# Performance work log

Hardware: AMD Instinct MI355X
Metric: run time of the kernel (lower is better)

## Reference

```python
import jax, jax.numpy as jnp
import numpy as np
import math

B, N, D, H, E, EDGE_DIM, GEO_DIM = 32, 256, 512, 8, 1024, 256, 64
HD = D // H

def _lin(x, W, b):
    return x @ W.T + b

def _ln(x, g, b):
    m = x.mean(-1, keepdims=True)
    v = ((x - m) ** 2).mean(-1, keepdims=True)
    return (x - m) * jax.lax.rsqrt(v + 1e-5) * g + b

def setup_inputs() -> dict:
    key = jax.random.key(0)
    ks = jax.random.split(key, 20)
    p = lambda k, s: jax.random.normal(k, s, jnp.float32) * 0.02
    inp = {
        'x': jax.random.normal(ks[0], (B, N, D), jnp.float32),
        'node_masks': jnp.ones((B, N), jnp.float32),
        'relation_edges': jax.random.randint(ks[1], (B, E, 2), 0, N),
        'relation_masks': (jax.random.uniform(ks[2], (B, E)) > 0.2).astype(jnp.float32),
        'relation_embeddings': jax.random.normal(ks[3], (B, E, EDGE_DIM), jnp.float32),
        'relation_geo_features': jax.random.normal(ks[4], (B, E, GEO_DIM), jnp.float32),
        'Wq': p(ks[5], (D, D)), 'bq': jnp.zeros((D,), jnp.float32),
        'Wk': p(ks[6], (D, D)), 'bk': jnp.zeros((D,), jnp.float32),
        'Wv': p(ks[7], (D, D)), 'bv': jnp.zeros((D,), jnp.float32),
        'W_eb': p(ks[8], (H, EDGE_DIM)), 'b_eb': jnp.zeros((H,), jnp.float32),
        'geo_ln_g': jnp.ones((GEO_DIM,), jnp.float32), 'geo_ln_b': jnp.zeros((GEO_DIM,), jnp.float32),
        'W_geo': p(ks[9], (H, GEO_DIM)), 'b_geo': jnp.zeros((H,), jnp.float32),
        'W_out': p(ks[10], (D, D)), 'b_out': jnp.zeros((D,), jnp.float32),
        'norm_g': jnp.ones((D,), jnp.float32), 'norm_b': jnp.zeros((D,), jnp.float32),
        'ff_ln_g': jnp.ones((D,), jnp.float32), 'ff_ln_b': jnp.zeros((D,), jnp.float32),
        'W_ff1': p(ks[11], (4 * D, D)), 'b_ff1': jnp.zeros((4 * D,), jnp.float32),
        'W_ff2': p(ks[12], (D, 4 * D)), 'b_ff2': jnp.zeros((D,), jnp.float32),
    }
    return inp

def reference(x, node_masks, relation_edges, relation_masks, relation_embeddings,
              relation_geo_features, Wq, bq, Wk, bk, Wv, bv, W_eb, b_eb,
              geo_ln_g, geo_ln_b, W_geo, b_geo, W_out, b_out, norm_g, norm_b,
              ff_ln_g, ff_ln_b, W_ff1, b_ff1, W_ff2, b_ff2):
    residual = x
    xn = _ln(x, norm_g, norm_b)
    q = _lin(xn, Wq, bq).reshape(B, N, H, HD)
    k = _lin(xn, Wk, bk).reshape(B, N, H, HD)
    v = _lin(xn, Wv, bv).reshape(B, N, H, HD)
    attn = jnp.einsum('bihd,bjhd->bhij', q, k) / math.sqrt(HD)

    nm = node_masks.astype(bool)
    pair_mask = nm[:, None, :, None] & nm[:, None, None, :]  # [B,1,N,N]

    valid = relation_masks.astype(bool)  # [B,E]
    idx = jnp.clip(relation_edges.astype(jnp.int32), 0, N - 1)
    src, dst = idx[..., 0], idx[..., 1]
    # route invalid edges to padding index N (sliced away after scatter)
    src_w = jnp.where(valid, src, N)
    dst_w = jnp.where(valid, dst, N)
    b_idx = jnp.broadcast_to(jnp.arange(B)[:, None], (B, E))

    adj = jnp.zeros((B, N + 1, N + 1), bool).at[:, :N, :N].set(jnp.eye(N, dtype=bool))
    adj = adj.at[b_idx, src_w, dst_w].set(True).at[b_idx, dst_w, src_w].set(True)
    rel_adj = adj[:, None, :N, :N]  # [B,1,N,N]

    eb = _lin(relation_embeddings, W_eb, b_eb)  # [B,E,H]
    gb = _lin(_ln(relation_geo_features, geo_ln_g, geo_ln_b), W_geo, b_geo)
    total_bias = (eb + gb).transpose(0, 2, 1)  # [B,H,E]
    bb = jnp.broadcast_to(b_idx[:, None, :], (B, H, E))
    hh = jnp.broadcast_to(jnp.arange(H)[None, :, None], (B, H, E))
    ss = jnp.broadcast_to(src_w[:, None, :], (B, H, E))
    dd = jnp.broadcast_to(dst_w[:, None, :], (B, H, E))
    rb = jnp.zeros((B, H, N + 1, N + 1), x.dtype)
    rb = rb.at[bb, hh, ss, dd].set(total_bias).at[bb, hh, dd, ss].set(total_bias)
    attn = attn + rb[:, :, :N, :N]

    mask = pair_mask & rel_adj
    attn = jnp.where(mask, attn, jnp.finfo(attn.dtype).min)
    attn = jnp.nan_to_num(jax.nn.softmax(attn, axis=-1))
    out = jnp.einsum('bhij,bjhd->bihd', attn, v).reshape(B, N, D)
    x2 = residual + _lin(out, W_out, b_out)
    h1 = jax.nn.silu(_lin(_ln(x2, ff_ln_g, ff_ln_b), W_ff1, b_ff1))
    x3 = x2 + _lin(h1, W_ff2, b_ff2)
    return x3 * node_masks[..., None]
```

## Files before the change

### kernel.cpp

```cpp
#include <hip/hip_runtime.h>

#define B_ 32
#define N_ 256
#define D_ 512
#define H_ 8
#define E_ 1024
#define HD_ 64

using u16 = unsigned short;
typedef short bf8_t __attribute__((ext_vector_type(8)));
typedef float f4_t __attribute__((ext_vector_type(4)));

__device__ __forceinline__ u16 f2bf(float f) {
  union { float f; unsigned u; } x; x.f = f;
  unsigned r = x.u + 0x7fffu + ((x.u >> 16) & 1u);
  return (u16)(r >> 16);
}
__device__ __forceinline__ float bf2f(u16 x) {
  union { unsigned u; float f; } y; y.u = ((unsigned)x) << 16; return y.f;
}
__device__ __forceinline__ f4_t mfma16(bf8_t a, bf8_t b, f4_t c) {
  return __builtin_amdgcn_mfma_f32_16x16x32_bf16(a, b, c, 0, 0, 0);
}
__device__ __forceinline__ void gload_lds16(const u16* g, u16* s) {
  __builtin_amdgcn_global_load_lds((const __attribute__((address_space(1))) void*)g,
                                   (__attribute__((address_space(3))) void*)s, 16, 0, 0);
}

__device__ __forceinline__ void ln_row_wave(const float* __restrict__ xr, int lane,
                                            const float* __restrict__ g,
                                            const float* __restrict__ bta,
                                            u16* __restrict__ outp) {
  const float4 a0 = *(const float4*)(xr + lane * 8);
  const float4 a1 = *(const float4*)(xr + lane * 8 + 4);
  float s  = a0.x + a0.y + a0.z + a0.w + a1.x + a1.y + a1.z + a1.w;
  float ss = a0.x * a0.x + a0.y * a0.y + a0.z * a0.z + a0.w * a0.w +
             a1.x * a1.x + a1.y * a1.y + a1.z * a1.z + a1.w * a1.w;
  #pragma unroll
  for (int m = 1; m < 64; m <<= 1) { s += __shfl_xor(s, m, 64); ss += __shfl_xor(ss, m, 64); }
  const float mean = s * (1.f / D_);
  const float rs = rsqrtf(ss * (1.f / D_) - mean * mean + 1e-5f);
  const float4 g0 = *(const float4*)(g + lane * 8);
  const float4 g1 = *(const float4*)(g + lane * 8 + 4);
  const float4 b0 = *(const float4*)(bta + lane * 8);
  const float4 b1 = *(const float4*)(bta + lane * 8 + 4);
  bf8_t res;
  res[0] = (short)f2bf((a0.x - mean) * rs * g0.x + b0.x);
  res[1] = (short)f2bf((a0.y - mean) * rs * g0.y + b0.y);
  res[2] = (short)f2bf((a0.z - mean) * rs * g0.z + b0.z);
  res[3] = (short)f2bf((a0.w - mean) * rs * g0.w + b0.w);
  res[4] = (short)f2bf((a1.x - mean) * rs * g1.x + b1.x);
  res[5] = (short)f2bf((a1.y - mean) * rs * g1.y + b1.y);
  res[6] = (short)f2bf((a1.z - mean) * rs * g1.z + b1.z);
  res[7] = (short)f2bf((a1.w - mean) * rs * g1.w + b1.w);
  *(bf8_t*)(outp + lane * 8) = res;
}

#define WEBP 264
#define WGEOP 72
__global__ __launch_bounds__(256) void prep_kernel(
    const float* __restrict__ wq, const float* __restrict__ wk,
    const float* __restrict__ wv, const float* __restrict__ wo,
    const float* __restrict__ w1, const float* __restrict__ w2,
    u16* __restrict__ dq, u16* __restrict__ dk, u16* __restrict__ dv,
    u16* __restrict__ dox, u16* __restrict__ d1, u16* __restrict__ d2,
    const float* __restrict__ x, const float* __restrict__ ng,
    const float* __restrict__ nb, u16* __restrict__ xn,
    const int* __restrict__ edges, const float* __restrict__ rmask,
    int* __restrict__ win,
    const float* __restrict__ remb, const float* __restrict__ rgeo,
    const float* __restrict__ Web, const float* __restrict__ beb,
    const float* __restrict__ glng, const float* __restrict__ glnb,
    const float* __restrict__ Wgeo, const float* __restrict__ bgeo,
    float* __restrict__ tb) {
  __shared__ u16 sWeb[16 * WEBP];
  __shared__ u16 sWgeo[16 * WGEOP];
  __shared__ float sLgb[128];
  const int t = threadIdx.x;
  const int blk0 = blockIdx.x;

  if (blk0 < 1536) {
    int blk = blk0;
    const float* src; u16* dst;
    if (blk < 128)        { src = wq; dst = dq; }
    else if (blk < 256)   { src = wk; dst = dk; blk -= 128; }
    else if (blk < 384)   { src = wv; dst = dv; blk -= 256; }
    else if (blk < 512)   { src = wo; dst = dox; blk -= 384; }
    else if (blk < 1024)  { src = w1; dst = d1; blk -= 512; }
    else                  { src = w2; dst = d2; blk -= 1024; }
    const int i = (blk * 256 + t) * 8;
    const float4 v0 = *(const float4*)(src + i);
    const float4 v1 = *(const float4*)(src + i + 4);
    bf8_t o;
    o[0] = (short)f2bf(v0.x); o[1] = (short)f2bf(v0.y);
    o[2] = (short)f2bf(v0.z); o[3] = (short)f2bf(v0.w);
    o[4] = (short)f2bf(v1.x); o[5] = (short)f2bf(v1.y);
    o[6] = (short)f2bf(v1.z); o[7] = (short)f2bf(v1.w);
    *(bf8_t*)(dst + i) = o;
  } else if (blk0 < 2560) {
    const int base = (blk0 - 1536) * 8 + (t >> 6) * 2;
    const int lane = t & 63;
    #pragma unroll
    for (int r = 0; r < 2; ++r) {
      const int row = base + r;
      ln_row_wave(x + (size_t)row * D_, lane, ng, nb, xn + (size_t)row * D_);
    }
  } else if (blk0 < 2688) {
    const int idx = (blk0 - 2560) * 256 + t;
    if (rmask[idx] != 0.f) {
      const int b = idx >> 10, e = idx & (E_ - 1);
      int s = edges[2 * idx], d = edges[2 * idx + 1];
      s = min(max(s, 0), N_ - 1);
      d = min(max(d, 0), N_ - 1);
      int* wb = win + (size_t)b * N_ * N_;
      atomicMax(&wb[s * N_ + d], e);
      atomicMax(&wb[d * N_ + s], E_ + e);
    }
  } else {
    const int eblk = blk0 - 2688;
    for (int i = t; i < 2048; i += 256) {
      const int r = i >> 8, c = i & 255;
      sWeb[r * WEBP + c] = f2bf(Web[i]);
      sWeb[(8 + r) * WEBP + c] = 0;
    }
    for (int i = t; i < 512; i += 256) {
      const int r = i >> 6, c = i & 63;
      sWgeo[r * WGEOP + c] = f2bf(Wgeo[i]);
      sWgeo[(8 + r) * WGEOP + c] = 0;
    }
    if (t < 64) { sLgb[t] = glng[t]; sLgb[64 + t] = glnb[t]; }
    __syncthreads();
    const int wave = t >> 6, lane = t & 63;
    const int am = lane & 15, quad = lane >> 4;
    const int e0 = eblk * 64 + wave * 16;

    f4_t acc = f4_t{0.f, 0.f, 0.f, 0.f};
    const float* ar = remb + (size_t)(e0 + am) * 256 + quad * 8;
    #pragma unroll
    for (int kt = 0; kt < 256; kt += 32) {
      const float4 p0 = *(const float4*)(ar + kt);
      const float4 p1 = *(const float4*)(ar + kt + 4);
      bf8_t a;
      a[0] = (short)f2bf(p0.x); a[1] = (short)f2bf(p0.y);
      a[2] = (short)f2bf(p0.z); a[3] = (short)f2bf(p0.w);
      a[4] = (short)f2bf(p1.x); a[5] = (short)f2bf(p1.y);
      a[6] = (short)f2bf(p1.z); a[7] = (short)f2bf(p1.w);
      const bf8_t bv = *(const bf8_t*)&sWeb[am * WEBP + kt + quad * 8];
      acc = mfma16(a, bv, acc);
    }
    const float* gr = rgeo + (size_t)(e0 + am) * 64;
    float v[16];
    {
      const float4 p0 = *(const float4*)(gr + quad * 8);
      const float4 p1 = *(const float4*)(gr + quad * 8 + 4);
      const float4 p2 = *(const float4*)(gr + 32 + quad * 8);
      const float4 p3 = *(const float4*)(gr + 32 + quad * 8 + 4);
      v[0] = p0.x; v[1] = p0.y; v[2] = p0.z; v[3] = p0.w;
      v[4] = p1.x; v[5] = p1.y; v[6] = p1.z; v[7] = p1.w;
      v[8] = p2.x; v[9] = p2.y; v[10] = p2.z; v[11] = p2.w;
      v[12] = p3.x; v[13] = p3.y; v[14] = p3.z; v[15] = p3.w;
    }
    float s = 0.f, ss = 0.f;
    #pragma unroll
    for (int j = 0; j < 16; ++j) { s += v[j]; ss += v[j] * v[j]; }
    s += __shfl_xor(s, 16, 64);  ss += __shfl_xor(ss, 16, 64);
    s += __shfl_xor(s, 32, 64);  ss += __shfl_xor(ss, 32, 64);
    const float mean = s * (1.f / 64.f);
    const float rs = rsqrtf(ss * (1.f / 64.f) - mean * mean + 1e-5f);
    bf8_t a2, a3;
    #pragma unroll
    for (int j = 0; j < 8; ++j) {
      a2[j] = (short)f2bf((v[j] - mean) * rs * sLgb[quad * 8 + j] + sLgb[64 + quad * 8 + j]);
      a3[j] = (short)f2bf((v[8 + j] - mean) * rs * sLgb[32 + quad * 8 + j] +
                          sLgb[96 + quad * 8 + j]);
    }
    acc = mfma16(a2, *(const bf8_t*)&sWgeo[am * WGEOP + quad * 8], acc);
    acc = mfma16(a3, *(const bf8_t*)&sWgeo[am * WGEOP + 32 + quad * 8], acc);
    if (am < 8) {
      const float bias_v = beb[am] + bgeo[am];
      #pragma unroll
      for (int r = 0; r < 4; ++r) {
        const int eg = e0 + quad * 4 + r;
        tb[(size_t)((eg >> 10) * H_ + am) * E_ + (eg & (E_ - 1))] = acc[r] + bias_v;
      }
    }
  }
}

__global__ __launch_bounds__(256) void ln_kernel(const float* __restrict__ x,
                                                 const float* __restrict__ g,
                                                 const float* __restrict__ bta,
                                                 u16* __restrict__ out) {
  const int base = blockIdx.x * 8 + (threadIdx.x >> 6) * 2;
  const int lane = threadIdx.x & 63;
  #pragma unroll
  for (int r = 0; r < 2; ++r) {
    const int row = base + r;
    ln_row_wave(x + (size_t)row * D_, lane, g, bta, out + (size_t)row * D_);
  }
}

__global__ __launch_bounds__(256) void attn_kernel(
    const u16* __restrict__ q, const u16* __restrict__ k, const u16* __restrict__ v,
    const float* __restrict__ tb, const int* __restrict__ win,
    const float* __restrict__ nm, u16* __restrict__ out) {
  const int t = threadIdx.x;
  const int wave = t >> 6, lane = t & 63;
  const int g = blockIdx.x * 4 + wave;
  const int b = g >> 8, row = g & (N_ - 1);
  u16* op = out + (size_t)g * D_ + lane * 8;
  const float nmr = nm[g];
  if (nmr == 0.f) {
    bf8_t z = 0;
    *(bf8_t*)op = z;
    return;
  }
  float qf[8];
  {
    const bf8_t qv = *(const bf8_t*)(q + (size_t)g * D_ + lane * 8);
    #pragma unroll
    for (int j = 0; j < 8; ++j) qf[j] = bf2f((u16)qv[j]);
  }
  int4 w4 = *(const int4*)(win + (size_t)g * N_ + lane * 4);
  if (lane == (row >> 2)) {
    const int sl = row & 3;
    if (sl == 0)      { if (w4.x == -1) w4.x = 0x7FFFFFFF; }
    else if (sl == 1) { if (w4.y == -1) w4.y = 0x7FFFFFFF; }
    else if (sl == 2) { if (w4.z == -1) w4.z = 0x7FFFFFFF; }
    else              { if (w4.w == -1) w4.w = 0x7FFFFFFF; }
  }
  const float* tbh = tb + (size_t)(b * H_ + (lane >> 3)) * E_;
  const float* nmb = nm + b * N_;
  const u16* kb = k + (size_t)b * N_ * D_;
  const u16* vb = v + (size_t)b * N_ * D_;
  float m = -3.402823466e38f, sum = 0.f;
  float o[8];
  #pragma unroll
  for (int j = 0; j < 8; ++j) o[j] = 0.f;
  #pragma unroll
  for (int c = 0; c < 4; ++c) {
    const int wc = (c == 0) ? w4.x : (c == 1) ? w4.y : (c == 2) ? w4.z : w4.w;
    unsigned long long mk = __ballot(wc != -1);
    while (mk) {
      const int jl = __builtin_ctzll(mk);
      mk &= mk - 1;
      const int col = jl * 4 + c;
      const int wv = __shfl(wc, jl, 64);
      const float nmc = nmb[col];
      if (nmc == 0.f) continue;
      const bf8_t kv = *(const bf8_t*)(kb + (size_t)col * D_ + lane * 8);
      float d = 0.f;
      #pragma unroll
      for (int j = 0; j < 8; ++j) d += qf[j] * bf2f((u16)kv[j]);
      d += __shfl_xor(d, 1, 64);
      d += __shfl_xor(d, 2, 64);
      d += __shfl_xor(d, 4, 64);
      float s = d * 0.125f;
      if ((unsigned)wv < 2048u) s += tbh[wv & (E_ - 1)];
      const bf8_t vv = *(const bf8_t*)(vb + (size_t)col * D_ + lane * 8);
      if (s > m) {
        const float sc = __expf(m - s);
        sum *= sc;
        #pragma unroll
        for (int j = 0; j < 8; ++j) o[j] *= sc;
        m = s;
      }
      const float p = __expf(s - m);
      sum += p;
      #pragma unroll
      for (int j = 0; j < 8; ++j) o[j] += p * bf2f((u16)vv[j]);
    }
  }
  const float rinv = 1.f / sum;
  bf8_t res;
  #pragma unroll
  for (int j = 0; j < 8; ++j) res[j] = (short)f2bf(o[j] * rinv);
  *(bf8_t*)op = res;
}

template <int MODE, int BN>
__global__ __launch_bounds__(256, 2) void gemm_k(
    const u16* __restrict__ A,
    const u16* __restrict__ W0, const u16* __restrict__ W1, const u16* __restrict__ W2,
    const float* __restrict__ b0, const float* __restrict__ b1, const float* __restrict__ b2,
    void* d0, void* d1, void* d2,
    const void* res, const float* __restrict__ nmask, int K) {
  constexpr int MJ = BN / 32;
  constexpr int CB = BN / 32;
  __shared__ u16 As[128 * 64];
  __shared__ u16 Bs[BN * 64];
  const int tid = threadIdx.x;
  const int wave = tid >> 6, lane = tid & 63;
  const int am = lane & 15, quad = lane >> 4;
  const int m0 = blockIdx.x * 128;
  int n0, proj = 0;
  const u16* W;
  const float* bias;
  if constexpr (MODE == 0) {
    constexpr int NPB = 512 / BN;
    proj = blockIdx.y / NPB;
    n0 = (blockIdx.y % NPB) * BN;
    W = proj == 0 ? W0 : (proj == 1 ? W1 : W2);
    bias = proj == 0 ? b0 : (proj == 1 ? b1 : b2);
  } else {
    n0 = blockIdx.y * BN;
    W = W0;
    bias = b0;
  }
  const int wm = (wave >> 1) * 64;
  const int wn = (wave & 1) * (BN / 2);

  f4_t acc[4][MJ];
  #pragma unroll
  for (int i = 0; i < 4; ++i)
    #pragma unroll
    for (int j = 0; j < MJ; ++j) acc[i][j] = f4_t{0.f, 0.f, 0.f, 0.f};

  int arow[4], aq[4], brow[CB], bq[CB];
  #pragma unroll
  for (int c = 0; c < 4; ++c) {
    const int g = (wave * 4 + c) * 64 + lane;
    arow[c] = g >> 3;
    aq[c] = (g & 7) ^ (arow[c] & 7);
  }
  #pragma unroll
  for (int c = 0; c < CB; ++c) {
    const int g = (wave * CB + c) * 64 + lane;
    brow[c] = g >> 3;
    bq[c] = (g & 7) ^ (brow[c] & 7);
  }

  for (int kt = 0; kt < K; kt += 64) {
    #pragma unroll
    for (int c = 0; c < 4; ++c)
      gload_lds16(A + (size_t)(m0 + arow[c]) * K + kt + aq[c] * 8, &As[(wave * 4 + c) * 512]);
    #pragma unroll
    for (int c = 0; c < CB; ++c)
      gload_lds16(W + (size_t)(n0 + brow[c]) * K + kt + bq[c] * 8, &Bs[(wave * CB + c) * 512]);
    __syncthreads();
    #pragma unroll
    for (int kc = 0; kc < 2; ++kc) {
      bf8_t af[4], bfv[MJ];
      #pragma unroll
      for (int i = 0; i < 4; ++i) {
        const int r = wm + i * 16 + am;
        af[i] = *(const bf8_t*)&As[r * 64 + (((kc * 4 + quad) ^ (r & 7)) * 8)];
      }
      #pragma unroll
      for (int j = 0; j < MJ; ++j) {
        const int r = wn + j * 16 + am;
        bfv[j] = *(const bf8_t*)&Bs[r * 64 + (((kc * 4 + quad) ^ (r & 7)) * 8)];
      }
      #pragma unroll
      for (int i = 0; i < 4; ++i)
        #pragma unroll
        for (int j = 0; j < MJ; ++j)
          acc[i][j] = mfma16(bfv[j], af[i], acc[i][j]);
    }
    __syncthreads();
  }

  const int row0 = m0 + wm + am;
  const int col0 = n0 + wn + quad * 4;
  #pragma unroll
  for (int j = 0; j < MJ; ++j) {
    const int col = col0 + j * 16;
    const float4 bv4 = *(const float4*)(bias + col);
    #pragma unroll
    for (int i = 0; i < 4; ++i) {
      const int row = row0 + i * 16;
      float v0 = acc[i][j][0] + bv4.x;
      float v1 = acc[i][j][1] + bv4.y;
      float v2 = acc[i][j][2] + bv4.z;
      float v3 = acc[i][j][3] + bv4.w;
      if constexpr (MODE == 0) {
        u16* dst = (u16*)(proj == 0 ? d0 : (proj == 1 ? d1 : d2));
        ushort4 o; o.x = f2bf(v0); o.y = f2bf(v1); o.z = f2bf(v2); o.w = f2bf(v3);
        *(ushort4*)(dst + (size_t)row * D_ + col) = o;
      } else if constexpr (MODE == 2) {
        const float4 rr = *(const float4*)((const float*)res + (size_t)row * D_ + col);
        float4 o; o.x = v0 + rr.x; o.y = v1 + rr.y; o.z = v2 + rr.z; o.w = v3 + rr.w;
        *(float4*)((float*)d0 + (size_t)row * D_ + col) = o;
      } else if constexpr (MODE == 3) {
        v0 = v0 / (1.f + __expf(-v0));
        v1 = v1 / (1.f + __expf(-v1));
        v2 = v2 / (1.f + __expf(-v2));
        v3 = v3 / (1.f + __expf(-v3));
        ushort4 o; o.x = f2bf(v0); o.y = f2bf(v1); o.z = f2bf(v2); o.w = f2bf(v3);
        *(ushort4*)((u16*)d0 + (size_t)row * 2048 + col) = o;
      } else {
        const float4 rr = *(const float4*)((const float*)res + (size_t)row * D_ + col);
        const float nmv = nmask[row];
        float4 o;
        o.x = (v0 + rr.x) * nmv; o.y = (v1 + rr.y) * nmv;
        o.z = (v2 + rr.z) * nmv; o.w = (v3 + rr.w) * nmv;
        *(float4*)((float*)d0 + (size_t)row * D_ + col) = o;
      }
    }
  }
}

extern "C" void kernel_launch(void* const* d_in, const int* in_sizes, int n_in,
                              void* d_out, int out_size, void* d_ws, size_t ws_size,
                              hipStream_t stream) {
  const float* x     = (const float*)d_in[0];
  const float* nm    = (const float*)d_in[1];
  const int*   edges = (const int*)d_in[2];
  const float* rmask = (const float*)d_in[3];
  const float* remb  = (const float*)d_in[4];
  const float* rgeo  = (const float*)d_in[5];
  const float* Wq = (const float*)d_in[6];  const float* bq = (const float*)d_in[7];
  const float* Wk = (const float*)d_in[8];  const float* bk = (const float*)d_in[9];
  const float* Wv = (const float*)d_in[10]; const float* bv = (const float*)d_in[11];
  const float* Web = (const float*)d_in[12]; const float* beb = (const float*)d_in[13];
  const float* glng = (const float*)d_in[14]; const float* glnb = (const float*)d_in[15];
  const float* Wgeo = (const float*)d_in[16]; const float* bgeo = (const float*)d_in[17];
  const float* Wout = (const float*)d_in[18]; const float* bout = (const float*)d_in[19];
  const float* ng = (const float*)d_in[20]; const float* nb = (const float*)d_in[21];
  const float* fg = (const float*)d_in[22]; const float* fb = (const float*)d_in[23];
  const float* Wff1 = (const float*)d_in[24]; const float* bff1 = (const float*)d_in[25];
  const float* Wff2 = (const float*)d_in[26]; const float* bff2 = (const float*)d_in[27];

  char* ws = (char*)d_ws;
  u16*   xn      = (u16*)(ws + 0);
  u16*   qb      = (u16*)(ws + 8388608);
  u16*   kb      = (u16*)(ws + 16777216);
  u16*   vb      = (u16*)(ws + 25165824);
  u16*   h1      = (u16*)(ws + 0);
  int*   win     = (int*)(ws + 33554432);
  u16*   x2n     = (u16*)(ws + 33554432);
  float* tb      = (float*)(ws + 41943040);
  u16* Wq16   = (u16*)(ws + 42991616);
  u16* Wk16   = (u16*)(ws + 43515904);
  u16* Wv16   = (u16*)(ws + 44040192);
  u16* Wout16 = (u16*)(ws + 44564480);
  u16* Wff116 = (u16*)(ws + 45088768);
  u16* Wff216 = (u16*)(ws + 47185920);
  u16*   attnout = xn;
  float* out     = (float*)d_out;

  hipMemsetAsync(win, 0xFF, (size_t)B_ * N_ * N_ * sizeof(int), stream);
  prep_kernel<<<3200, 256, 0, stream>>>(
      Wq, Wk, Wv, Wout, Wff1, Wff2, Wq16, Wk16, Wv16, Wout16, Wff116, Wff216,
      x, ng, nb, xn,
      edges, rmask, win,
      remb, rgeo, Web, beb, glng, glnb, Wgeo, bgeo, tb);
  gemm_k<0, 128><<<dim3(64, 12), 256, 0, stream>>>(xn, Wq16, Wk16, Wv16, bq, bk, bv,
                                                   (void*)qb, (void*)kb, (void*)vb,
                                                   nullptr, nullptr, D_);
  attn_kernel<<<dim3(B_ * N_ / 4), 256, 0, stream>>>(qb, kb, vb, tb, win, nm, attnout);
  gemm_k<2, 64><<<dim3(64, 8), 256, 0, stream>>>(attnout, Wout16, nullptr, nullptr,
                                                 bout, nullptr, nullptr,
                                                 (void*)out, nullptr, nullptr,
                                                 (const void*)x, nullptr, D_);
  ln_kernel<<<B_ * N_ / 8, 256, 0, stream>>>(out, fg, fb, x2n);
  gemm_k<3, 128><<<dim3(64, 16), 256, 0, stream>>>(x2n, Wff116, nullptr, nullptr,
                                                   bff1, nullptr, nullptr,
                                                   (void*)h1, nullptr, nullptr, nullptr, nullptr, D_);
  gemm_k<4, 64><<<dim3(64, 8), 256, 0, stream>>>(h1, Wff216, nullptr, nullptr,
                                                 bff2, nullptr, nullptr,
                                                 (void*)out, nullptr, nullptr,
                                                 (const void*)out, nm, 2048);
}
```

Baseline: 284.4 us.

## Triple-buffer GEMM tiles with async global-to-LDS prefetch and smaller 64x64 tiles

Reworks the shared GEMM kernel into a three-stage LDS ring. Tiles two k-steps ahead are issued with direct global-to-LDS loads and waited on with explicit vmcnt counts and raw barriers, replacing the load-sync-compute-sync loop. Block tiles shrink to 64 rows (and 64 columns for all projections), and launch bounds now target three blocks per CU. The aim is to hide memory latency and raise occupancy and grid size, at the cost of less operand reuse per tile and fragile hand-counted waitcnt values.

```diff
diff --git a/kernel.cpp b/kernel.cpp
--- a/kernel.cpp
+++ b/kernel.cpp
@@ -279,7 +279,7 @@
 }
 
 template <int MODE, int BN>
-__global__ __launch_bounds__(256, 2) void gemm_k(
+__global__ __launch_bounds__(256, 3) void gemm_k(
     const u16* __restrict__ A,
     const u16* __restrict__ W0, const u16* __restrict__ W1, const u16* __restrict__ W2,
     const float* __restrict__ b0, const float* __restrict__ b1, const float* __restrict__ b2,
@@ -287,12 +287,12 @@
     const void* res, const float* __restrict__ nmask, int K) {
   constexpr int MJ = BN / 32;
   constexpr int CB = BN / 32;
-  __shared__ u16 As[128 * 64];
-  __shared__ u16 Bs[BN * 64];
+  __shared__ u16 As[3][64 * 64];
+  __shared__ u16 Bs[3][BN * 64];
   const int tid = threadIdx.x;
   const int wave = tid >> 6, lane = tid & 63;
   const int am = lane & 15, quad = lane >> 4;
-  const int m0 = blockIdx.x * 128;
+  const int m0 = blockIdx.x * 64;
   int n0, proj = 0;
   const u16* W;
   const float* bias;
@@ -307,19 +307,19 @@
     W = W0;
     bias = b0;
   }
-  const int wm = (wave >> 1) * 64;
+  const int wm = (wave >> 1) * 32;
   const int wn = (wave & 1) * (BN / 2);
 
-  f4_t acc[4][MJ];
-  #pragma unroll
-  for (int i = 0; i < 4; ++i)
+  f4_t acc[2][MJ];
+  #pragma unroll
+  for (int i = 0; i < 2; ++i)
     #pragma unroll
     for (int j = 0; j < MJ; ++j) acc[i][j] = f4_t{0.f, 0.f, 0.f, 0.f};
 
-  int arow[4], aq[4], brow[CB], bq[CB];
-  #pragma unroll
-  for (int c = 0; c < 4; ++c) {
-    const int g = (wave * 4 + c) * 64 + lane;
+  int arow[2], aq[2], brow[CB], bq[CB];
+  #pragma unroll
+  for (int c = 0; c < 2; ++c) {
+    const int g = (wave * 2 + c) * 64 + lane;
     arow[c] = g >> 3;
     aq[c] = (g & 7) ^ (arow[c] & 7);
   }
@@ -330,34 +330,55 @@
     bq[c] = (g & 7) ^ (brow[c] & 7);
   }
 
-  for (int kt = 0; kt < K; kt += 64) {
-    #pragma unroll
-    for (int c = 0; c < 4; ++c)
-      gload_lds16(A + (size_t)(m0 + arow[c]) * K + kt + aq[c] * 8, &As[(wave * 4 + c) * 512]);
+  const int nsteps = K >> 6;
+  auto STAGE = [&](int s, int buf) {
+    const int kt = s * 64;
+    #pragma unroll
+    for (int c = 0; c < 2; ++c)
+      gload_lds16(A + (size_t)(m0 + arow[c]) * K + kt + aq[c] * 8,
+                  &As[buf][(wave * 2 + c) * 512]);
     #pragma unroll
     for (int c = 0; c < CB; ++c)
-      gload_lds16(W + (size_t)(n0 + brow[c]) * K + kt + bq[c] * 8, &Bs[(wave * CB + c) * 512]);
-    __syncthreads();
+      gload_lds16(W + (size_t)(n0 + brow[c]) * K + kt + bq[c] * 8,
+                  &Bs[buf][(wave * CB + c) * 512]);
+  };
+
+  STAGE(0, 0);
+  if (nsteps > 1) STAGE(1, 1);
+
+  int cur = 0;
+  for (int t = 0; t < nsteps; ++t) {
+    int nxt2 = cur + 2; if (nxt2 >= 3) nxt2 -= 3;
+    if (t + 2 < nsteps) {
+      STAGE(t + 2, nxt2);
+      asm volatile("s_waitcnt vmcnt(8)" ::: "memory");
+    } else if (t + 1 < nsteps) {
+      asm volatile("s_waitcnt vmcnt(4)" ::: "memory");
+    } else {
+      asm volatile("s_waitcnt vmcnt(0)" ::: "memory");
+    }
+    asm volatile("s_barrier" ::: "memory");
     #pragma unroll
     for (int kc = 0; kc < 2; ++kc) {
-      bf8_t af[4], bfv[MJ];
-      #pragma unroll
-      for (int i = 0; i < 4; ++i) {
+      bf8_t af[2], bfv[MJ];
+      #pragma unroll
+      for (int i = 0; i < 2; ++i) {
         const int r = wm + i * 16 + am;
-        af[i] = *(const bf8_t*)&As[r * 64 + (((kc * 4 + quad) ^ (r & 7)) * 8)];
+        af[i] = *(const bf8_t*)&As[cur][r * 64 + (((kc * 4 + quad) ^ (r & 7)) * 8)];
       }
       #pragma unroll
       for (int j = 0; j < MJ; ++j) {
         const int r = wn + j * 16 + am;
-        bfv[j] = *(const bf8_t*)&Bs[r * 64 + (((kc * 4 + quad) ^ (r & 7)) * 8)];
+        bfv[j] = *(const bf8_t*)&Bs[cur][r * 64 + (((kc * 4 + quad) ^ (r & 7)) * 8)];
       }
       #pragma unroll
-      for (int i = 0; i < 4; ++i)
+      for (int i = 0; i < 2; ++i)
         #pragma unroll
         for (int j = 0; j < MJ; ++j)
           acc[i][j] = mfma16(bfv[j], af[i], acc[i][j]);
     }
-    __syncthreads();
+    asm volatile("s_barrier" ::: "memory");
+    ++cur; if (cur >= 3) cur = 0;
   }
 
   const int row0 = m0 + wm + am;
@@ -367,7 +388,7 @@
     const int col = col0 + j * 16;
     const float4 bv4 = *(const float4*)(bias + col);
     #pragma unroll
-    for (int i = 0; i < 4; ++i) {
+    for (int i = 0; i < 2; ++i) {
       const int row = row0 + i * 16;
       float v0 = acc[i][j][0] + bv4.x;
       float v1 = acc[i][j][1] + bv4.y;
@@ -445,20 +466,20 @@
       x, ng, nb, xn,
       edges, rmask, win,
       remb, rgeo, Web, beb, glng, glnb, Wgeo, bgeo, tb);
-  gemm_k<0, 128><<<dim3(64, 12), 256, 0, stream>>>(xn, Wq16, Wk16, Wv16, bq, bk, bv,
+  gemm_k<0, 64><<<dim3(128, 24), 256, 0, stream>>>(xn, Wq16, Wk16, Wv16, bq, bk, bv,
                                                    (void*)qb, (void*)kb, (void*)vb,
                                                    nullptr, nullptr, D_);
   attn_kernel<<<dim3(B_ * N_ / 4), 256, 0, stream>>>(qb, kb, vb, tb, win, nm, attnout);
-  gemm_k<2, 64><<<dim3(64, 8), 256, 0, stream>>>(attnout, Wout16, nullptr, nullptr,
-                                                 bout, nullptr, nullptr,
-                                                 (void*)out, nullptr, nullptr,
-                                                 (const void*)x, nullptr, D_);
+  gemm_k<2, 64><<<dim3(128, 8), 256, 0, stream>>>(attnout, Wout16, nullptr, nullptr,
+                                                  bout, nullptr, nullptr,
+                                                  (void*)out, nullptr, nullptr,
+                                                  (const void*)x, nullptr, D_);
   ln_kernel<<<B_ * N_ / 8, 256, 0, stream>>>(out, fg, fb, x2n);
-  gemm_k<3, 128><<<dim3(64, 16), 256, 0, stream>>>(x2n, Wff116, nullptr, nullptr,
+  gemm_k<3, 64><<<dim3(128, 32), 256, 0, stream>>>(x2n, Wff116, nullptr, nullptr,
                                                    bff1, nullptr, nullptr,
                                                    (void*)h1, nullptr, nullptr, nullptr, nullptr, D_);
-  gemm_k<4, 64><<<dim3(64, 8), 256, 0, stream>>>(h1, Wff216, nullptr, nullptr,
-                                                 bff2, nullptr, nullptr,
-                                                 (void*)out, nullptr, nullptr,
-                                                 (const void*)out, nm, 2048);
-}
+  gemm_k<4, 64><<<dim3(128, 8), 256, 0, stream>>>(h1, Wff216, nullptr, nullptr,
+                                                  bff2, nullptr, nullptr,
+                                                  (void*)out, nullptr, nullptr,
+                                                  (const void*)out, nm, 2048);
+}
```

Measured after the change: 327.5 us. +15.2%, slower.

## Add 256x256-tile double-buffered GEMM kernel for QKV and FF1 projections

Applied to the files above, without the earlier changes.

Adds a new 512-thread GEMM kernel with 256x256 output tiles, double-buffered LDS staging and raised wave priority around the MFMA loop, and uses it for the fused QKV projection and the FF1+SiLU projection. The larger tiles raise arithmetic intensity per loaded byte, and the double buffering overlaps global loads with compute. The old gemm_k is narrowed to the out-projection and FF2 modes. The cost is 128 KB of LDS per block and far fewer blocks (192 and 256), which risks poor CU occupancy and load balance on a many-CU GPU.

```diff
diff --git a/kernel.cpp b/kernel.cpp
--- a/kernel.cpp
+++ b/kernel.cpp
@@ -278,12 +278,131 @@
   *(bf8_t*)op = res;
 }
 
+template <int MODE>
+__global__ __launch_bounds__(512, 2) void gemm256_k(
+    const u16* __restrict__ A,
+    const u16* __restrict__ W0, const u16* __restrict__ W1, const u16* __restrict__ W2,
+    const float* __restrict__ b0, const float* __restrict__ b1, const float* __restrict__ b2,
+    void* d0, void* d1, void* d2, int K) {
+  __shared__ u16 As[2][256 * 64];
+  __shared__ u16 Bs[2][256 * 64];
+  const int tid = threadIdx.x;
+  const int wave = tid >> 6, lane = tid & 63;
+  const int am = lane & 15, quad = lane >> 4;
+  const int m0 = blockIdx.x * 256;
+  int n0, proj = 0;
+  const u16* W;
+  const float* bias;
+  if constexpr (MODE == 0) {
+    proj = blockIdx.y >> 1;
+    n0 = (blockIdx.y & 1) * 256;
+    W = proj == 0 ? W0 : (proj == 1 ? W1 : W2);
+    bias = proj == 0 ? b0 : (proj == 1 ? b1 : b2);
+  } else {
+    n0 = blockIdx.y * 256;
+    W = W0;
+    bias = b0;
+  }
+  const int wm = (wave >> 2) * 128;
+  const int wn = (wave & 3) * 64;
+
+  f4_t acc[8][4];
+  #pragma unroll
+  for (int i = 0; i < 8; ++i)
+    #pragma unroll
+    for (int j = 0; j < 4; ++j) acc[i][j] = f4_t{0.f, 0.f, 0.f, 0.f};
+
+  int srow[4], sq[4];
+  #pragma unroll
+  for (int c = 0; c < 4; ++c) {
+    const int g = c * 512 + tid;
+    srow[c] = g >> 3;
+    sq[c] = (g & 7) ^ (srow[c] & 7);
+  }
+
+  const int nt = K >> 6;
+  #pragma unroll
+  for (int c = 0; c < 4; ++c) {
+    gload_lds16(A + (size_t)(m0 + srow[c]) * K + sq[c] * 8, &As[0][c * 4096 + wave * 512]);
+    gload_lds16(W + (size_t)(n0 + srow[c]) * K + sq[c] * 8, &Bs[0][c * 4096 + wave * 512]);
+  }
+  asm volatile("s_waitcnt vmcnt(0)" ::: "memory");
+  asm volatile("s_barrier" ::: "memory");
+
+  int cur = 0;
+  for (int t = 0; t < nt; ++t) {
+    const int nxt = cur ^ 1;
+    if (t + 1 < nt) {
+      const int kt = (t + 1) * 64;
+      #pragma unroll
+      for (int c = 0; c < 4; ++c) {
+        gload_lds16(A + (size_t)(m0 + srow[c]) * K + kt + sq[c] * 8,
+                    &As[nxt][c * 4096 + wave * 512]);
+        gload_lds16(W + (size_t)(n0 + srow[c]) * K + kt + sq[c] * 8,
+                    &Bs[nxt][c * 4096 + wave * 512]);
+      }
+    }
+    __builtin_amdgcn_s_setprio(1);
+    #pragma unroll
+    for (int kc = 0; kc < 2; ++kc) {
+      bf8_t af[8], bfv[4];
+      #pragma unroll
+      for (int i = 0; i < 8; ++i) {
+        const int r = wm + i * 16 + am;
+        af[i] = *(const bf8_t*)&As[cur][r * 64 + (((kc * 4 + quad) ^ (r & 7)) * 8)];
+      }
+      #pragma unroll
+      for (int j = 0; j < 4; ++j) {
+        const int r = wn + j * 16 + am;
+        bfv[j] = *(const bf8_t*)&Bs[cur][r * 64 + (((kc * 4 + quad) ^ (r & 7)) * 8)];
+      }
+      #pragma unroll
+      for (int i = 0; i < 8; ++i)
+        #pragma unroll
+        for (int j = 0; j < 4; ++j)
+          acc[i][j] = mfma16(bfv[j], af[i], acc[i][j]);
+    }
+    __builtin_amdgcn_s_setprio(0);
+    asm volatile("s_waitcnt vmcnt(0)" ::: "memory");
+    asm volatile("s_barrier" ::: "memory");
+    cur = nxt;
+  }
+
+  const int row0 = m0 + wm + am;
+  const int col0 = n0 + wn + quad * 4;
+  #pragma unroll
+  for (int j = 0; j < 4; ++j) {
+    const int col = col0 + j * 16;
+    const float4 bv4 = *(const float4*)(bias + col);
+    #pragma unroll
+    for (int i = 0; i < 8; ++i) {
+      const int row = row0 + i * 16;
+      float v0 = acc[i][j][0] + bv4.x;
+      float v1 = acc[i][j][1] + bv4.y;
+      float v2 = acc[i][j][2] + bv4.z;
+      float v3 = acc[i][j][3] + bv4.w;
+      if constexpr (MODE == 0) {
+        u16* dst = (u16*)(proj == 0 ? d0 : (proj == 1 ? d1 : d2));
+        ushort4 o; o.x = f2bf(v0); o.y = f2bf(v1); o.z = f2bf(v2); o.w = f2bf(v3);
+        *(ushort4*)(dst + (size_t)row * D_ + col) = o;
+      } else {
+        v0 = v0 / (1.f + __expf(-v0));
+        v1 = v1 / (1.f + __expf(-v1));
+        v2 = v2 / (1.f + __expf(-v2));
+        v3 = v3 / (1.f + __expf(-v3));
+        ushort4 o; o.x = f2bf(v0); o.y = f2bf(v1); o.z = f2bf(v2); o.w = f2bf(v3);
+        *(ushort4*)((u16*)d0 + (size_t)row * 2048 + col) = o;
+      }
+    }
+  }
+}
+
 template <int MODE, int BN>
 __global__ __launch_bounds__(256, 2) void gemm_k(
     const u16* __restrict__ A,
-    const u16* __restrict__ W0, const u16* __restrict__ W1, const u16* __restrict__ W2,
-    const float* __restrict__ b0, const float* __restrict__ b1, const float* __restrict__ b2,
-    void* d0, void* d1, void* d2,
+    const u16* __restrict__ W0,
+    const float* __restrict__ b0,
+    void* d0,
     const void* res, const float* __restrict__ nmask, int K) {
   constexpr int MJ = BN / 32;
   constexpr int CB = BN / 32;
@@ -293,20 +412,9 @@
   const int wave = tid >> 6, lane = tid & 63;
   const int am = lane & 15, quad = lane >> 4;
   const int m0 = blockIdx.x * 128;
-  int n0, proj = 0;
-  const u16* W;
-  const float* bias;
-  if constexpr (MODE == 0) {
-    constexpr int NPB = 512 / BN;
-    proj = blockIdx.y / NPB;
-    n0 = (blockIdx.y % NPB) * BN;
-    W = proj == 0 ? W0 : (proj == 1 ? W1 : W2);
-    bias = proj == 0 ? b0 : (proj == 1 ? b1 : b2);
-  } else {
-    n0 = blockIdx.y * BN;
-    W = W0;
-    bias = b0;
-  }
+  const int n0 = blockIdx.y * BN;
+  const u16* W = W0;
+  const float* bias = b0;
   const int wm = (wave >> 1) * 64;
   const int wn = (wave & 1) * (BN / 2);
 
@@ -373,21 +481,10 @@
       float v1 = acc[i][j][1] + bv4.y;
       float v2 = acc[i][j][2] + bv4.z;
       float v3 = acc[i][j][3] + bv4.w;
-      if constexpr (MODE == 0) {
-        u16* dst = (u16*)(proj == 0 ? d0 : (proj == 1 ? d1 : d2));
-        ushort4 o; o.x = f2bf(v0); o.y = f2bf(v1); o.z = f2bf(v2); o.w = f2bf(v3);
-        *(ushort4*)(dst + (size_t)row * D_ + col) = o;
-      } else if constexpr (MODE == 2) {
+      if constexpr (MODE == 2) {
         const float4 rr = *(const float4*)((const float*)res + (size_t)row * D_ + col);
         float4 o; o.x = v0 + rr.x; o.y = v1 + rr.y; o.z = v2 + rr.z; o.w = v3 + rr.w;
         *(float4*)((float*)d0 + (size_t)row * D_ + col) = o;
-      } else if constexpr (MODE == 3) {
-        v0 = v0 / (1.f + __expf(-v0));
-        v1 = v1 / (1.f + __expf(-v1));
-        v2 = v2 / (1.f + __expf(-v2));
-        v3 = v3 / (1.f + __expf(-v3));
-        ushort4 o; o.x = f2bf(v0); o.y = f2bf(v1); o.z = f2bf(v2); o.w = f2bf(v3);
-        *(ushort4*)((u16*)d0 + (size_t)row * 2048 + col) = o;
       } else {
         const float4 rr = *(const float4*)((const float*)res + (size_t)row * D_ + col);
         const float nmv = nmask[row];
@@ -445,20 +542,15 @@
       x, ng, nb, xn,
       edges, rmask, win,
       remb, rgeo, Web, beb, glng, glnb, Wgeo, bgeo, tb);
-  gemm_k<0, 128><<<dim3(64, 12), 256, 0, stream>>>(xn, Wq16, Wk16, Wv16, bq, bk, bv,
-                                                   (void*)qb, (void*)kb, (void*)vb,
-                                                   nullptr, nullptr, D_);
+  gemm256_k<0><<<dim3(32, 6), 512, 0, stream>>>(xn, Wq16, Wk16, Wv16, bq, bk, bv,
+                                                (void*)qb, (void*)kb, (void*)vb, D_);
   attn_kernel<<<dim3(B_ * N_ / 4), 256, 0, stream>>>(qb, kb, vb, tb, win, nm, attnout);
-  gemm_k<2, 64><<<dim3(64, 8), 256, 0, stream>>>(attnout, Wout16, nullptr, nullptr,
-                                                 bout, nullptr, nullptr,
-                                                 (void*)out, nullptr, nullptr,
-                                                 (const void*)x, nullptr, D_);
+  gemm_k<2, 64><<<dim3(64, 8), 256, 0, stream>>>(attnout, Wout16, bout,
+                                                 (void*)out, (const void*)x, nullptr, D_);
   ln_kernel<<<B_ * N_ / 8, 256, 0, stream>>>(out, fg, fb, x2n);
-  gemm_k<3, 128><<<dim3(64, 16), 256, 0, stream>>>(x2n, Wff116, nullptr, nullptr,
-                                                   bff1, nullptr, nullptr,
-                                                   (void*)h1, nullptr, nullptr, nullptr, nullptr, D_);
-  gemm_k<4, 64><<<dim3(64, 8), 256, 0, stream>>>(h1, Wff216, nullptr, nullptr,
-                                                 bff2, nullptr, nullptr,
-                                                 (void*)out, nullptr, nullptr,
-                                                 (const void*)out, nm, 2048);
-}
+  gemm256_k<3><<<dim3(32, 8), 512, 0, stream>>>(x2n, Wff116, nullptr, nullptr,
+                                                bff1, nullptr, nullptr,
+                                                (void*)h1, nullptr, nullptr, D_);
+  gemm_k<4, 64><<<dim3(64, 8), 256, 0, stream>>>(h1, Wff216, bff2,
+                                                 (void*)out, (const void*)out, nm, 2048);
+}
```

Measured after the change: 294.7 us. 3.6% more time.
